# Kernel tuning notes

Measured on AMD Instinct MI355X. Metric: run time of the kernel, lower is better.

## Reference

```python
import jax, jax.numpy as jnp
import numpy as np

B, N, D = 4, 2048, 4
COUPLING = 1.0
DT = 1.0


def setup_inputs() -> dict:
    key = jax.random.key(0)
    k1, k2, k3, k4 = jax.random.split(key, 4)
    theta_prev = jax.random.normal(k1, (B, N, D), dtype=jnp.float32)
    gamma_t = jax.random.normal(k2, (B, N, D), dtype=jnp.float32)
    affinity = jax.random.uniform(k3, (B, N, N), dtype=jnp.float32)
    alpha_t = jax.random.normal(k4, (B, N, N), dtype=jnp.float32)
    # learned parameters, initialized as in the torch module
    omega = jnp.zeros((N, D), dtype=jnp.float32)
    kappa = jnp.ones((N, D), dtype=jnp.float32)
    alpha_bias = jnp.zeros((N, N), dtype=jnp.float32)
    return {
        "theta_prev": theta_prev,
        "gamma_t": gamma_t,
        "affinity": affinity,
        "alpha_t": alpha_t,
        "omega": omega,
        "kappa": kappa,
        "alpha_bias": alpha_bias,
    }


def reference(theta_prev, gamma_t, affinity, alpha_t, omega, kappa, alpha_bias):
    # theta_prev: [B, N, D], affinity/alpha_t: [B, N, N]
    n = theta_prev.shape[1]
    alpha_total = alpha_t + alpha_bias[None, :, :]               # [B, N, N]
    # phase_term[b, i, j, d] = sin(theta[b, j, d] - theta[b, i, d] - alpha_total[b, i, j])
    phase_term = jnp.sin(
        theta_prev[:, None, :, :] - theta_prev[:, :, None, :]
        - alpha_total[:, :, :, None]
    )                                                            # [B, N, N, D]
    coupling_term = (COUPLING / n) * jnp.einsum(
        "bij,bijd->bid", affinity, phase_term
    )                                                            # [B, N, D]
    drive_term = kappa[None, :, :] * (gamma_t - theta_prev)
    theta_dot = omega[None, :, :] + drive_term + coupling_term
    return theta_prev + DT * theta_dot
```

## Files before the change

kernel.cpp:

```cpp
#include <hip/hip_runtime.h>

#define BB 4
#define NN 2048
#define DD 4
#define QQ (NN / 4)
#define BLOCK 256
#define JIT (QQ / 64)

typedef float f4 __attribute__((ext_vector_type(4)));
typedef _Float16 h8 __attribute__((ext_vector_type(8)));
typedef _Float16 h2 __attribute__((ext_vector_type(2)));

#if __has_builtin(__builtin_amdgcn_fdot2) && __has_builtin(__builtin_amdgcn_cvt_pkrtz)
#define USE_FDOT2 1
#endif

__global__ __launch_bounds__(BLOCK) void precomp(const float* __restrict__ theta,
                                                 float* __restrict__ sArr,
                                                 float* __restrict__ cArr,
                                                 h8* __restrict__ scT) {
    const int t = blockIdx.x * BLOCK + threadIdx.x;
    const int b = t / QQ, q = t % QQ;
    const f4* theta4 = (const f4*)theta;
    f4* s4 = (f4*)sArr;
    f4* c4 = (f4*)cArr;

    float s[4][4], c[4][4];
    #pragma unroll
    for (int u = 0; u < 4; ++u) {
        const f4 th = theta4[(size_t)b * NN + 4 * q + u];
        #pragma unroll
        for (int d = 0; d < 4; ++d) __sincosf(th[d], &s[u][d], &c[u][d]);
    }
    #pragma unroll
    for (int u = 0; u < 4; ++u) {
        f4 sv, cv;
        #pragma unroll
        for (int d = 0; d < 4; ++d) { sv[d] = s[u][d]; cv[d] = c[u][d]; }
        s4[(size_t)b * NN + 4 * q + u] = sv;
        c4[(size_t)b * NN + 4 * q + u] = cv;
    }
    #pragma unroll
    for (int d = 0; d < 4; ++d) {
        h8 w;
        #pragma unroll
        for (int u = 0; u < 4; ++u) {
            w[2 * u]     = (_Float16)s[u][d];
            w[2 * u + 1] = (_Float16)c[u][d];
        }
        scT[((size_t)b * 4 + d) * QQ + q] = w;
    }
}

__global__ __launch_bounds__(BLOCK, 5) void kuramoto_main(
    const float* __restrict__ theta,
    const float* __restrict__ gam,
    const float* __restrict__ aff,
    const float* __restrict__ alp,
    const float* __restrict__ omega,
    const float* __restrict__ kappa,
    const float* __restrict__ bias,
    const float* __restrict__ sArr,
    const float* __restrict__ cArr,
    const uint4* __restrict__ scT,
    float* __restrict__ out)
{
    const int x   = blockIdx.x;
    const int low = x & 31;
    const int b   = low >> 3;
    const int g   = (x >> 5) * 8 + (low & 7);
    const int i0  = g * 4;

    const int tid  = threadIdx.x;
    const int wave = tid >> 6;
    const int lane = tid & 63;
    const int i    = i0 + wave;

    __shared__ uint4 lsc[4 * QQ];
    {
        const uint4* gsc = scT + (size_t)b * 4 * QQ;
        #pragma unroll
        for (int k = 0; k < (4 * QQ) / BLOCK; ++k)
            lsc[tid + BLOCK * k] = gsc[tid + BLOCK * k];
    }
    __syncthreads();

    const f4* arow = (const f4*)(aff + (size_t)b * NN * NN) + (size_t)i * QQ;
    const f4* lrow = (const f4*)(alp + (size_t)b * NN * NN) + (size_t)i * QQ;
    const f4* brow = (const f4*)bias + (size_t)i * QQ;

    f4 accU = {0.f, 0.f, 0.f, 0.f};
    f4 accV = {0.f, 0.f, 0.f, 0.f};

    f4 av[2], lv[2], bv[2];
    av[0] = __builtin_nontemporal_load(&arow[lane]);
    lv[0] = __builtin_nontemporal_load(&lrow[lane]);
    bv[0] = brow[lane];

    #pragma unroll
    for (int jj = 0; jj < JIT; ++jj) {
        const int cur = jj & 1;
        const int nxt = cur ^ 1;
        const int q   = lane + 64 * jj;

        if (jj + 1 < JIT) {
            const int qn = q + 64;
            av[nxt] = __builtin_nontemporal_load(&arow[qn]);
            lv[nxt] = __builtin_nontemporal_load(&lrow[qn]);
            bv[nxt] = brow[qn];
        }

        const uint4 w0 = lsc[0 * QQ + q];
        const uint4 w1 = lsc[1 * QQ + q];
        const uint4 w2 = lsc[2 * QQ + q];
        const uint4 w3 = lsc[3 * QQ + q];
        const unsigned wq[4][4] = {
            {w0.x, w0.y, w0.z, w0.w},
            {w1.x, w1.y, w1.z, w1.w},
            {w2.x, w2.y, w2.z, w2.w},
            {w3.x, w3.y, w3.z, w3.w},
        };

        const f4 alr = lv[cur] + bv[cur];
        const f4 af  = av[cur];
        #pragma unroll
        for (int u = 0; u < 4; ++u) {
            float sa, ca;
            __sincosf(alr[u], &sa, &ca);
            const float wc = af[u] * ca;
            const float ws = af[u] * sa;
#ifdef USE_FDOT2
            const h2 pw = __builtin_bit_cast(h2, __builtin_amdgcn_cvt_pkrtz(wc, -ws));
            const h2 pv = __builtin_bit_cast(h2, __builtin_amdgcn_cvt_pkrtz(ws,  wc));
            #pragma unroll
            for (int d = 0; d < 4; ++d) {
                const h2 pr = __builtin_bit_cast(h2, wq[d][u]);
                accU[d] = __builtin_amdgcn_fdot2(pw, pr, accU[d], false);
                accV[d] = __builtin_amdgcn_fdot2(pv, pr, accV[d], false);
            }
#else
            #pragma unroll
            for (int d = 0; d < 4; ++d) {
                const h2 pr = __builtin_bit_cast(h2, wq[d][u]);
                const float sj = (float)pr[0];
                const float cj = (float)pr[1];
                accU[d] += wc * sj - ws * cj;
                accV[d] += wc * cj + ws * sj;
            }
#endif
        }
    }

    #pragma unroll
    for (int off = 32; off >= 1; off >>= 1) {
        #pragma unroll
        for (int d = 0; d < 4; ++d) {
            accU[d] += __shfl_down(accU[d], off, 64);
            accV[d] += __shfl_down(accV[d], off, 64);
        }
    }

    if (lane == 0) {
        const f4* theta4 = (const f4*)theta;
        const f4* gam4   = (const f4*)gam;
        const f4* om4    = (const f4*)omega;
        const f4* kp4    = (const f4*)kappa;
        const f4* s4     = (const f4*)sArr;
        const f4* c4     = (const f4*)cArr;
        f4* out4         = (f4*)out;

        const size_t base = (size_t)b * NN + i;
        const f4 th = theta4[base];
        const f4 gm = gam4[base];
        const f4 om = om4[i];
        const f4 kp = kp4[i];
        const f4 si = s4[base];
        const f4 ci = c4[base];
        f4 o;
        #pragma unroll
        for (int d = 0; d < 4; ++d) {
            const float coup = (1.0f / (float)NN) * (ci[d] * accU[d] - si[d] * accV[d]);
            o[d] = th[d] + om[d] + kp[d] * (gm[d] - th[d]) + coup;
        }
        out4[base] = o;
    }
}

extern "C" void kernel_launch(void* const* d_in, const int* in_sizes, int n_in,
                              void* d_out, int out_size, void* d_ws, size_t ws_size,
                              hipStream_t stream) {
    const float* theta = (const float*)d_in[0];
    const float* gam   = (const float*)d_in[1];
    const float* aff   = (const float*)d_in[2];
    const float* alp   = (const float*)d_in[3];
    const float* omega = (const float*)d_in[4];
    const float* kappa = (const float*)d_in[5];
    const float* bias  = (const float*)d_in[6];
    float* out  = (float*)d_out;

    float* sArr = (float*)d_ws;
    float* cArr = sArr + BB * NN * DD;
    h8*    scT  = (h8*)(cArr + BB * NN * DD);

    precomp<<<(BB * QQ) / BLOCK, BLOCK, 0, stream>>>(theta, sArr, cArr, scT);
    kuramoto_main<<<BB * (NN / 4), BLOCK, 0, stream>>>(
        theta, gam, aff, alp, omega, kappa, bias, sArr, cArr, (const uint4*)scT, out);
}
```

Before: 169.1 us.

## Fuse sin/cos precompute into main kernel, recomputing per block into LDS

Drops the separate precompute kernel and its workspace arrays. Each block now computes sin/cos of theta for its batch straight into shared memory, and the final combine recomputes sin/cos of theta_i. This removes one kernel launch and a global round trip. In exchange, every one of the 2048 blocks repeats 2048×4 sincos evaluations, adding ALU work before the barrier, though the first affinity/alpha loads are issued early to overlap with it.

```diff
diff --git a/kernel.cpp b/kernel.cpp
--- a/kernel.cpp
+++ b/kernel.cpp
@@ -8,51 +8,22 @@
 #define JIT (QQ / 64)
 
 typedef float f4 __attribute__((ext_vector_type(4)));
-typedef _Float16 h8 __attribute__((ext_vector_type(8)));
 typedef _Float16 h2 __attribute__((ext_vector_type(2)));
 
 #if __has_builtin(__builtin_amdgcn_fdot2) && __has_builtin(__builtin_amdgcn_cvt_pkrtz)
 #define USE_FDOT2 1
 #endif
 
-__global__ __launch_bounds__(BLOCK) void precomp(const float* __restrict__ theta,
-                                                 float* __restrict__ sArr,
-                                                 float* __restrict__ cArr,
-                                                 h8* __restrict__ scT) {
-    const int t = blockIdx.x * BLOCK + threadIdx.x;
-    const int b = t / QQ, q = t % QQ;
-    const f4* theta4 = (const f4*)theta;
-    f4* s4 = (f4*)sArr;
-    f4* c4 = (f4*)cArr;
-
-    float s[4][4], c[4][4];
-    #pragma unroll
-    for (int u = 0; u < 4; ++u) {
-        const f4 th = theta4[(size_t)b * NN + 4 * q + u];
-        #pragma unroll
-        for (int d = 0; d < 4; ++d) __sincosf(th[d], &s[u][d], &c[u][d]);
-    }
-    #pragma unroll
-    for (int u = 0; u < 4; ++u) {
-        f4 sv, cv;
-        #pragma unroll
-        for (int d = 0; d < 4; ++d) { sv[d] = s[u][d]; cv[d] = c[u][d]; }
-        s4[(size_t)b * NN + 4 * q + u] = sv;
-        c4[(size_t)b * NN + 4 * q + u] = cv;
-    }
-    #pragma unroll
-    for (int d = 0; d < 4; ++d) {
-        h8 w;
-        #pragma unroll
-        for (int u = 0; u < 4; ++u) {
-            w[2 * u]     = (_Float16)s[u][d];
-            w[2 * u + 1] = (_Float16)c[u][d];
-        }
-        scT[((size_t)b * 4 + d) * QQ + q] = w;
-    }
+static __device__ __forceinline__ unsigned pack_sc(float s, float c) {
+#ifdef USE_FDOT2
+    return __builtin_bit_cast(unsigned, __builtin_amdgcn_cvt_pkrtz(s, c));
+#else
+    h2 p; p[0] = (_Float16)s; p[1] = (_Float16)c;
+    return __builtin_bit_cast(unsigned, p);
+#endif
 }
 
-__global__ __launch_bounds__(BLOCK, 5) void kuramoto_main(
+__global__ __launch_bounds__(BLOCK, 5) void kuramoto_fused(
     const float* __restrict__ theta,
     const float* __restrict__ gam,
     const float* __restrict__ aff,
@@ -60,9 +31,6 @@
     const float* __restrict__ omega,
     const float* __restrict__ kappa,
     const float* __restrict__ bias,
-    const float* __restrict__ sArr,
-    const float* __restrict__ cArr,
-    const uint4* __restrict__ scT,
     float* __restrict__ out)
 {
     const int x   = blockIdx.x;
@@ -76,26 +44,41 @@
     const int lane = tid & 63;
     const int i    = i0 + wave;
 
-    __shared__ uint4 lsc[4 * QQ];
-    {
-        const uint4* gsc = scT + (size_t)b * 4 * QQ;
-        #pragma unroll
-        for (int k = 0; k < (4 * QQ) / BLOCK; ++k)
-            lsc[tid + BLOCK * k] = gsc[tid + BLOCK * k];
-    }
-    __syncthreads();
-
     const f4* arow = (const f4*)(aff + (size_t)b * NN * NN) + (size_t)i * QQ;
     const f4* lrow = (const f4*)(alp + (size_t)b * NN * NN) + (size_t)i * QQ;
     const f4* brow = (const f4*)bias + (size_t)i * QQ;
-
-    f4 accU = {0.f, 0.f, 0.f, 0.f};
-    f4 accV = {0.f, 0.f, 0.f, 0.f};
 
     f4 av[2], lv[2], bv[2];
     av[0] = __builtin_nontemporal_load(&arow[lane]);
     lv[0] = __builtin_nontemporal_load(&lrow[lane]);
     bv[0] = brow[lane];
+
+    __shared__ uint4 lsc[4 * QQ];
+    const f4* theta4 = (const f4*)theta + (size_t)b * NN;
+    #pragma unroll
+    for (int k = 0; k < QQ / BLOCK; ++k) {
+        const int q = tid + BLOCK * k;
+        float s[4][4], c[4][4];
+        #pragma unroll
+        for (int u = 0; u < 4; ++u) {
+            const f4 th = theta4[4 * q + u];
+            #pragma unroll
+            for (int d = 0; d < 4; ++d) __sincosf(th[d], &s[u][d], &c[u][d]);
+        }
+        #pragma unroll
+        for (int d = 0; d < 4; ++d) {
+            uint4 w;
+            w.x = pack_sc(s[0][d], c[0][d]);
+            w.y = pack_sc(s[1][d], c[1][d]);
+            w.z = pack_sc(s[2][d], c[2][d]);
+            w.w = pack_sc(s[3][d], c[3][d]);
+            lsc[d * QQ + q] = w;
+        }
+    }
+    __syncthreads();
+
+    f4 accU = {0.f, 0.f, 0.f, 0.f};
+    f4 accV = {0.f, 0.f, 0.f, 0.f};
 
     #pragma unroll
     for (int jj = 0; jj < JIT; ++jj) {
@@ -161,25 +144,22 @@
     }
 
     if (lane == 0) {
-        const f4* theta4 = (const f4*)theta;
-        const f4* gam4   = (const f4*)gam;
-        const f4* om4    = (const f4*)omega;
-        const f4* kp4    = (const f4*)kappa;
-        const f4* s4     = (const f4*)sArr;
-        const f4* c4     = (const f4*)cArr;
-        f4* out4         = (f4*)out;
+        const f4* gam4 = (const f4*)gam;
+        const f4* om4  = (const f4*)omega;
+        const f4* kp4  = (const f4*)kappa;
+        f4* out4       = (f4*)out;
 
         const size_t base = (size_t)b * NN + i;
-        const f4 th = theta4[base];
+        const f4 th = theta4[i];
         const f4 gm = gam4[base];
         const f4 om = om4[i];
         const f4 kp = kp4[i];
-        const f4 si = s4[base];
-        const f4 ci = c4[base];
         f4 o;
         #pragma unroll
         for (int d = 0; d < 4; ++d) {
-            const float coup = (1.0f / (float)NN) * (ci[d] * accU[d] - si[d] * accV[d]);
+            float si, ci;
+            __sincosf(th[d], &si, &ci);
+            const float coup = (1.0f / (float)NN) * (ci * accU[d] - si * accV[d]);
             o[d] = th[d] + om[d] + kp[d] * (gm[d] - th[d]) + coup;
         }
         out4[base] = o;
@@ -197,12 +177,8 @@
     const float* kappa = (const float*)d_in[5];
     const float* bias  = (const float*)d_in[6];
     float* out  = (float*)d_out;
+    (void)d_ws; (void)ws_size;
 
-    float* sArr = (float*)d_ws;
-    float* cArr = sArr + BB * NN * DD;
-    h8*    scT  = (h8*)(cArr + BB * NN * DD);
-
-    precomp<<<(BB * QQ) / BLOCK, BLOCK, 0, stream>>>(theta, sArr, cArr, scT);
-    kuramoto_main<<<BB * (NN / 4), BLOCK, 0, stream>>>(
-        theta, gam, aff, alp, omega, kappa, bias, sArr, cArr, (const uint4*)scT, out);
+    kuramoto_fused<<<BB * (NN / 4), BLOCK, 0, stream>>>(
+        theta, gam, aff, alp, omega, kappa, bias, out);
 }
```

After: 167.0 us. Within noise of the previous version (-1.2%).
